# Kernel tuning notes

Measured on AMD Instinct MI355X. Metric: run time of the kernel, lower is better.

The kernel has to match this reference:

```python
import jax, jax.numpy as jnp
import numpy as np

DIM = 1024
N_HEADS = 16
HD = DIM // N_HEADS


def setup_inputs() -> dict:
    key = jax.random.key(0)
    k1, k2, k3 = jax.random.split(key, 3)
    x = jax.random.normal(k1, (4, 2048, DIM), dtype=jnp.float32)
    # torch nn.Linear weights: W_qkv [3*dim, dim], W_proj [dim, dim]; y = x @ W.T
    W_qkv = jax.random.normal(k2, (3 * DIM, DIM), dtype=jnp.float32) * 0.02
    W_proj = jax.random.normal(k3, (DIM, DIM), dtype=jnp.float32) * 0.02
    return {"x": x, "W_qkv": W_qkv, "W_proj": W_proj}


def reference(x, W_qkv, W_proj):
    B, T, D = x.shape
    H, hd = N_HEADS, HD
    # fused QKV projection: (B,T,3D)
    qkv = jnp.einsum('btd,ed->bte', x, W_qkv)
    # view(B,T,3,H,hd).transpose(1,2) -> (B,3,T,H,hd)
    qkv = qkv.reshape(B, T, 3, H, hd).transpose(0, 2, 1, 3, 4)
    q, k, v = qkv[:, 0], qkv[:, 1], qkv[:, 2]  # each (B,T,H,hd)
    # NOTE: faithful to source — SDPA sees (B,T) as batch dims and attends
    # over the heads axis (length H), NOT the sequence axis.
    scale = 1.0 / np.sqrt(hd).astype(np.float32)
    scores = jnp.einsum('btie,btje->btij', q, k) * scale  # (B,T,H,H)
    attn = jax.nn.softmax(scores, axis=-1)
    out = jnp.einsum('btij,btje->btie', attn, v)  # (B,T,H,hd)
    # out.transpose(1,2).contiguous().view(B,T,D)
    out = out.transpose(0, 2, 1, 3).reshape(B, T, D)
    return jnp.einsum('btd,ed->bte', out, W_proj)
```

## Files before the change

kernel.cpp:

```cpp
#include <hip/hip_runtime.h>


typedef __bf16 bf16x8 __attribute__((ext_vector_type(8)));
typedef float  f32x16 __attribute__((ext_vector_type(16)));

typedef __attribute__((address_space(3))) void       lds_void;
typedef const __attribute__((address_space(1))) void gbl_void;

__device__ __forceinline__ unsigned short f2b(float f) {
    unsigned int u = __builtin_bit_cast(unsigned int, f);
    return (unsigned short)((u + 0x7FFFu + ((u >> 16) & 1u)) >> 16);
}
__device__ __forceinline__ unsigned int pack2(float a, float b) {
    return (unsigned int)f2b(a) | ((unsigned int)f2b(b) << 16);
}
__device__ __forceinline__ void unpack8(uint4 u, float* f) {
    unsigned int w[4] = {u.x, u.y, u.z, u.w};
#pragma unroll
    for (int a = 0; a < 4; ++a) {
        union { unsigned int i; float f; } lo, hi;
        lo.i = w[a] << 16;
        hi.i = w[a] & 0xFFFF0000u;
        f[a * 2]     = lo.f;
        f[a * 2 + 1] = hi.f;
    }
}

__global__ __launch_bounds__(256) void cvt_all(const float* __restrict__ x,
                                               const float* __restrict__ wqkv,
                                               const float* __restrict__ wproj,
                                               unsigned short* __restrict__ xb,
                                               unsigned short* __restrict__ wqkvb,
                                               unsigned short* __restrict__ wprojb) {
    int i = blockIdx.x * 256 + threadIdx.x;
    const float* src;
    unsigned short* dst;
    if (i < 2097152)      { src = x;     dst = xb;                   }
    else if (i < 2883584) { src = wqkv;  dst = wqkvb;  i -= 2097152; }
    else                  { src = wproj; dst = wprojb; i -= 2883584; }
    float4 f = reinterpret_cast<const float4*>(src)[i];
    ushort4 u;
    u.x = f2b(f.x); u.y = f2b(f.y); u.z = f2b(f.z); u.w = f2b(f.w);
    reinterpret_cast<ushort4*>(dst)[i] = u;
}

__device__ __forceinline__ void store_c(float* C, long idx, float v)          { C[idx] = v; }
__device__ __forceinline__ void store_c(unsigned short* C, long idx, float v) { C[idx] = f2b(v); }

template <int BM, int BN, typename CT>
__global__ __launch_bounds__(256, 3) void gemm_bt(const unsigned short* __restrict__ A,
                                                  const unsigned short* __restrict__ B,
                                                  CT* __restrict__ C,
                                                  int M, int N, int K) {
    constexpr int MI = BM / 64;
    constexpr int NJ = BN / 64;
    __shared__ __align__(16) unsigned short As[BM * 64];
    __shared__ __align__(16) unsigned short Bs[BN * 64];

    const int tid  = threadIdx.x;
    const int lane = tid & 63;
    const int wave = tid >> 6;
    const long bm  = blockIdx.y;
    const long bn  = blockIdx.x;
    const int wm   = (wave >> 1) * (BM / 2);
    const int wn   = (wave & 1) * (BN / 2);

    f32x16 acc[MI][NJ] = {};

    const unsigned short* Ab = A + bm * BM * (long)K;
    const unsigned short* Bb = B + bn * BN * (long)K;

    const int srow  = tid >> 3;
    const int sgcol = ((tid & 7) ^ (srow & 7)) << 3;

    for (int k0 = 0; k0 < K; k0 += 64) {
#pragma unroll
        for (int r = 0; r < BM / 32; ++r)
            __builtin_amdgcn_global_load_lds(
                (gbl_void*)(Ab + (long)(r * 32 + srow) * K + k0 + sgcol),
                (lds_void*)(As + (r * 256 + wave * 64) * 8), 16, 0, 0);
#pragma unroll
        for (int r = 0; r < BN / 32; ++r)
            __builtin_amdgcn_global_load_lds(
                (gbl_void*)(Bb + (long)(r * 32 + srow) * K + k0 + sgcol),
                (lds_void*)(Bs + (r * 256 + wave * 64) * 8), 16, 0, 0);
        __syncthreads();

        const int arow = lane & 31;
        const int kh   = lane >> 5;
#pragma unroll
        for (int kk = 0; kk < 4; ++kk) {
            const int c  = kk * 2 + kh;
            const int sw = (c ^ (lane & 7)) << 3;
            bf16x8 af[MI], bfr[NJ];
#pragma unroll
            for (int i = 0; i < MI; ++i)
                af[i] = *reinterpret_cast<const bf16x8*>(As + (wm + i * 32 + arow) * 64 + sw);
#pragma unroll
            for (int j = 0; j < NJ; ++j)
                bfr[j] = *reinterpret_cast<const bf16x8*>(Bs + (wn + j * 32 + arow) * 64 + sw);
#pragma unroll
            for (int i = 0; i < MI; ++i)
#pragma unroll
                for (int j = 0; j < NJ; ++j)
                    acc[i][j] = __builtin_amdgcn_mfma_f32_32x32x16_bf16(af[i], bfr[j], acc[i][j], 0, 0, 0);
        }
        __syncthreads();
    }

    const long mbase = bm * BM + wm + ((lane >> 5) << 2);
    const long nbase = bn * BN + wn + (lane & 31);
#pragma unroll
    for (int i = 0; i < MI; ++i)
#pragma unroll
        for (int j = 0; j < NJ; ++j)
#pragma unroll
            for (int r = 0; r < 16; ++r) {
                const long row = mbase + i * 32 + (r & 3) + 8 * (r >> 2);
                store_c(C, row * (long)N + nbase + j * 32, acc[i][j][r]);
            }
}

__global__ __launch_bounds__(256) void attn_rowlocal(const unsigned short* __restrict__ qkv,
                                                     unsigned short* __restrict__ out3) {
    __shared__ __align__(16) unsigned short rows[4 * 3072];
    __shared__ float attnS[4][16][17];

    const int tid  = threadIdx.x;
    const int lane = tid & 63;
    const int wave = tid >> 6;
    const int m0   = blockIdx.x * 4;

    {
        const uint4* src = reinterpret_cast<const uint4*>(qkv + (long)m0 * 3072);
        uint4* dst = reinterpret_cast<uint4*>(rows);
#pragma unroll
        for (int c = 0; c < 6; ++c) {
            const int S  = c * 256 + tid;
            const int gs = (S & ~7) | ((S & 7) ^ ((S >> 3) & 7));
            dst[S] = src[gs];
        }
    }
    __syncthreads();

    const int m = m0 + wave;
    const int b = m >> 11;
    const int t = m & 2047;
    const unsigned short* rw = rows + wave * 3072;

    const int i  = lane & 15;
    const int j0 = (lane >> 4) << 2;
    float sc[4] = {0.f, 0.f, 0.f, 0.f};
#pragma unroll
    for (int c8 = 0; c8 < 8; ++c8) {
        uint4 qu = *reinterpret_cast<const uint4*>(rw + i * 64 + ((c8 ^ (i & 7)) << 3));
        float qf[8];
        unpack8(qu, qf);
#pragma unroll
        for (int jj = 0; jj < 4; ++jj) {
            const int vi = 16 + j0 + jj;
            uint4 ku = *reinterpret_cast<const uint4*>(rw + vi * 64 + ((c8 ^ (vi & 7)) << 3));
            float kf[8];
            unpack8(ku, kf);
#pragma unroll
            for (int d = 0; d < 8; ++d) sc[jj] += qf[d] * kf[d];
        }
    }
#pragma unroll
    for (int jj = 0; jj < 4; ++jj) sc[jj] *= 0.125f;

    float mx = fmaxf(fmaxf(sc[0], sc[1]), fmaxf(sc[2], sc[3]));
    mx = fmaxf(mx, __shfl_xor(mx, 16));
    mx = fmaxf(mx, __shfl_xor(mx, 32));
    float sum = 0.f;
#pragma unroll
    for (int jj = 0; jj < 4; ++jj) { sc[jj] = __expf(sc[jj] - mx); sum += sc[jj]; }
    sum += __shfl_xor(sum, 16);
    sum += __shfl_xor(sum, 32);
    const float inv = 1.0f / sum;
#pragma unroll
    for (int jj = 0; jj < 4; ++jj) attnS[wave][i][j0 + jj] = sc[jj] * inv;
    __syncthreads();

    const int oi = lane >> 2;
    const int s0 = (lane & 3) << 4;
    const int c0 = (lane & 3) << 1;
    float o[16];
#pragma unroll
    for (int ss = 0; ss < 16; ++ss) o[ss] = 0.f;
#pragma unroll
    for (int j = 0; j < 16; ++j) {
        const float a  = attnS[wave][oi][j];
        const int   vi = 32 + j;
        uint4 v0 = *reinterpret_cast<const uint4*>(rw + vi * 64 + (((c0)     ^ (vi & 7)) << 3));
        uint4 v1 = *reinterpret_cast<const uint4*>(rw + vi * 64 + (((c0 + 1) ^ (vi & 7)) << 3));
        float vf[16];
        unpack8(v0, vf);
        unpack8(v1, vf + 8);
#pragma unroll
        for (int ss = 0; ss < 16; ++ss) o[ss] += a * vf[ss];
    }

    uint4 r0, r1;
    r0.x = pack2(o[0],  o[1]);  r0.y = pack2(o[2],  o[3]);
    r0.z = pack2(o[4],  o[5]);  r0.w = pack2(o[6],  o[7]);
    r1.x = pack2(o[8],  o[9]);  r1.y = pack2(o[10], o[11]);
    r1.z = pack2(o[12], o[13]); r1.w = pack2(o[14], o[15]);

    const long base = (long)b * (2048 * 1024)
                    + (long)(oi * 128 + (t >> 4)) * 1024
                    + 64 * (t & 15) + s0;
    *reinterpret_cast<uint4*>(out3 + base)     = r0;
    *reinterpret_cast<uint4*>(out3 + base + 8) = r1;
}

extern "C" void kernel_launch(void* const* d_in, const int* in_sizes, int n_in,
                              void* d_out, int out_size, void* d_ws, size_t ws_size,
                              hipStream_t stream) {
    const float* x     = (const float*)d_in[0];
    const float* Wqkv  = (const float*)d_in[1];
    const float* Wproj = (const float*)d_in[2];
    float* out = (float*)d_out;

    char* ws = (char*)d_ws;
    unsigned short* xb     = (unsigned short*)(ws);
    unsigned short* wqkvb  = (unsigned short*)(ws + 16777216);
    unsigned short* wprojb = (unsigned short*)(ws + 23068672);
    unsigned short* qkvb   = (unsigned short*)(ws + 25165824);
    unsigned short* out3b  = (unsigned short*)(ws + 75497472);

    cvt_all<<<dim3(12288), dim3(256), 0, stream>>>(x, Wqkv, Wproj, xb, wqkvb, wprojb);

    gemm_bt<128, 256, unsigned short><<<dim3(12, 64), dim3(256), 0, stream>>>(
        xb, wqkvb, qkvb, 8192, 3072, 1024);

    attn_rowlocal<<<dim3(2048), dim3(256), 0, stream>>>(qkvb, out3b);

    gemm_bt<64, 128, float><<<dim3(8, 128), dim3(256), 0, stream>>>(
        out3b, wprojb, out, 8192, 1024, 1024);
}
```

Before: 197.2 us.

## Replace QKV GEMM with 256x256 ping-pong pipelined 8-wave kernel

```diff
diff --git a/kernel.cpp b/kernel.cpp
--- a/kernel.cpp
+++ b/kernel.cpp
@@ -3,6 +3,7 @@
 
 typedef __bf16 bf16x8 __attribute__((ext_vector_type(8)));
 typedef float  f32x16 __attribute__((ext_vector_type(16)));
+typedef float  f32x4  __attribute__((ext_vector_type(4)));
 
 typedef __attribute__((address_space(3))) void       lds_void;
 typedef const __attribute__((address_space(1))) void gbl_void;
@@ -47,11 +48,138 @@
 __device__ __forceinline__ void store_c(float* C, long idx, float v)          { C[idx] = v; }
 __device__ __forceinline__ void store_c(unsigned short* C, long idx, float v) { C[idx] = f2b(v); }
 
+#define BAR   __builtin_amdgcn_s_barrier()
+#define LGKM0 asm volatile("s_waitcnt lgkmcnt(0)" ::: "memory")
+#define LGKM8 asm volatile("s_waitcnt lgkmcnt(8)" ::: "memory")
+#define VM4   asm volatile("s_waitcnt vmcnt(4)" ::: "memory")
+
+template <typename CT>
+__global__ __launch_bounds__(512, 2) void gemm256p(const unsigned short* __restrict__ A,
+                                                   const unsigned short* __restrict__ B,
+                                                   CT* __restrict__ C,
+                                                   int M, int N, int K, int NBX) {
+    __shared__ __align__(16) unsigned short sA[2][16384];
+    __shared__ __align__(16) unsigned short sB[2][16384];
+
+    const int tid  = threadIdx.x;
+    const int lane = tid & 63;
+    const int wave = tid >> 6;
+    const int wm   = wave >> 2;
+    const int wn   = wave & 3;
+
+    const int nwg = gridDim.x;
+    const int cpx = nwg >> 3;
+    const int swz = (blockIdx.x & 7) * cpx + (blockIdx.x >> 3);
+    const long bm = swz / NBX;
+    const long bn = swz % NBX;
+
+    const unsigned short* Ab = A + bm * 256 * (long)K;
+    const unsigned short* Bb = B + bn * 256 * (long)K;
+
+    f32x4 acc[8][4] = {};
+
+    auto stage = [&](const unsigned short* __restrict__ G, unsigned short* L,
+                     int tile, int half) {
+        const int r = tid >> 3;
+        const int c = ((tid & 7) ^ (r & 7)) << 3;
+        const unsigned short* g = G + (long)(half * 128 + r) * K + (long)tile * 64 + c;
+        unsigned short* l = L + half * 8192 + wave * 512;
+#pragma unroll
+        for (int j = 0; j < 2; ++j)
+            __builtin_amdgcn_global_load_lds((gbl_void*)(g + (long)j * 64 * K),
+                                             (lds_void*)(l + j * 4096), 16, 0, 0);
+    };
+
+    stage(Bb, &sB[0][0], 0, 0); stage(Bb, &sB[0][0], 0, 1);
+    stage(Ab, &sA[0][0], 0, 0); stage(Ab, &sA[0][0], 0, 1);
+    stage(Bb, &sB[1][0], 1, 0); stage(Bb, &sB[1][0], 1, 1);
+    VM4;
+    BAR;
+
+    const int fr = lane & 15;
+    const int fk = lane >> 4;
+    const int sx = lane & 7;
+
+    bf16x8 af[4][2], b01[2][2], b23[2][2];
+
+    auto read_a4 = [&](int q, int mbase) {
+#pragma unroll
+        for (int mt = 0; mt < 4; ++mt) {
+            const int row = wm * 128 + (mbase + mt) * 16 + fr;
+#pragma unroll
+            for (int h = 0; h < 2; ++h)
+                af[mt][h] = *reinterpret_cast<const bf16x8*>(
+                    &sA[q][row * 64 + (((h * 4 + fk) ^ sx) << 3)]);
+        }
+    };
+    auto read_b2 = [&](int q, int nbase, bf16x8 (&bf)[2][2]) {
+#pragma unroll
+        for (int nt = 0; nt < 2; ++nt) {
+            const int row = wn * 64 + (nbase + nt) * 16 + fr;
+#pragma unroll
+            for (int h = 0; h < 2; ++h)
+                bf[nt][h] = *reinterpret_cast<const bf16x8*>(
+                    &sB[q][row * 64 + (((h * 4 + fk) ^ sx) << 3)]);
+        }
+    };
+    auto mmq = [&](int mbase, int nbase, bf16x8 (&bf)[2][2]) {
+        __builtin_amdgcn_s_setprio(1);
+#pragma unroll
+        for (int mt = 0; mt < 4; ++mt)
+#pragma unroll
+            for (int nt = 0; nt < 2; ++nt)
+#pragma unroll
+                for (int h = 0; h < 2; ++h)
+                    acc[mbase + mt][nbase + nt] = __builtin_amdgcn_mfma_f32_16x16x32_bf16(
+                        af[mt][h], bf[nt][h], acc[mbase + mt][nbase + nt], 0, 0, 0);
+        __builtin_amdgcn_s_setprio(0);
+    };
+
+    const int NITER = K >> 7;
+    for (int it = 0; it < NITER; ++it) {
+        const int u = it * 2;
+        read_a4(0, 0); read_b2(0, 0, b01);
+        stage(Ab, &sA[1][0], u + 1, 0);
+        LGKM8; BAR; LGKM0; mmq(0, 0, b01); BAR;
+        read_b2(0, 2, b23);
+        stage(Ab, &sA[1][0], u + 1, 1);
+        BAR; LGKM0; mmq(0, 2, b23); BAR;
+        read_a4(0, 4);
+        stage(Bb, &sB[0][0], u + 2, 0);
+        BAR; LGKM0; mmq(4, 2, b23); BAR;
+        stage(Bb, &sB[0][0], u + 2, 1);
+        BAR; mmq(4, 0, b01); BAR;
+        VM4;
+        read_a4(1, 0); read_b2(1, 0, b01);
+        stage(Ab, &sA[0][0], u + 2, 0);
+        LGKM8; BAR; LGKM0; mmq(0, 0, b01); BAR;
+        read_b2(1, 2, b23);
+        stage(Ab, &sA[0][0], u + 2, 1);
+        BAR; LGKM0; mmq(0, 2, b23); BAR;
+        read_a4(1, 4);
+        stage(Bb, &sB[1][0], u + 3, 0);
+        BAR; LGKM0; mmq(4, 2, b23); BAR;
+        stage(Bb, &sB[1][0], u + 3, 1);
+        BAR; mmq(4, 0, b01); BAR;
+        VM4;
+    }
+
+    const long mb = bm * 256 + wm * 128 + (fk << 2);
+    const long nb = bn * 256 + wn * 64 + fr;
+#pragma unroll
+    for (int mt = 0; mt < 8; ++mt)
+#pragma unroll
+        for (int nt = 0; nt < 4; ++nt)
+#pragma unroll
+            for (int r = 0; r < 4; ++r)
+                store_c(C, (mb + mt * 16 + r) * (long)N + nb + nt * 16, acc[mt][nt][r]);
+}
+
 template <int BM, int BN, typename CT>
-__global__ __launch_bounds__(256, 3) void gemm_bt(const unsigned short* __restrict__ A,
-                                                  const unsigned short* __restrict__ B,
-                                                  CT* __restrict__ C,
-                                                  int M, int N, int K) {
+__global__ __launch_bounds__(256) void gemm_bt(const unsigned short* __restrict__ A,
+                                               const unsigned short* __restrict__ B,
+                                               CT* __restrict__ C,
+                                               int M, int N, int K) {
     constexpr int MI = BM / 64;
     constexpr int NJ = BN / 64;
     __shared__ __align__(16) unsigned short As[BM * 64];
@@ -231,8 +359,8 @@
 
     cvt_all<<<dim3(12288), dim3(256), 0, stream>>>(x, Wqkv, Wproj, xb, wqkvb, wprojb);
 
-    gemm_bt<128, 256, unsigned short><<<dim3(12, 64), dim3(256), 0, stream>>>(
-        xb, wqkvb, qkvb, 8192, 3072, 1024);
+    gemm256p<unsigned short><<<dim3(384), dim3(512), 0, stream>>>(
+        xb, wqkvb, qkvb, 8192, 3072, 1024, 12);
 
     attn_rowlocal<<<dim3(2048), dim3(256), 0, stream>>>(qkvb, out3b);
 
```

New measurement: 211.7 us. 7.4% more time.
